# Performance work log

Hardware: AMD Instinct MI355X
Metric: run time of the kernel (lower is better)

Reference implementation:

```python
import jax, jax.numpy as jnp
import numpy as np


def hard_sigmoid(x):
    # clamp(0.2*x + 0.5, 0, 1) -- Theano/lwtnn convention
    return jnp.clip(0.2 * x + 0.5, 0.0, 1.0)


def setup_inputs() -> dict:
    key = jax.random.key(0)
    ks = jax.random.split(key, 10)
    B, T, D, H = 128, 1024, 256, 256
    s_in = 1.0 / np.sqrt(D)
    s_h = 1.0 / np.sqrt(H)
    return {
        "x": jax.random.normal(ks[0], (B, T, D), dtype=jnp.float32),
        "W_z": jax.random.normal(ks[1], (D, H), dtype=jnp.float32) * s_in,
        "W_r": jax.random.normal(ks[2], (D, H), dtype=jnp.float32) * s_in,
        "W_h": jax.random.normal(ks[3], (D, H), dtype=jnp.float32) * s_in,
        "U_z": jax.random.normal(ks[4], (H, H), dtype=jnp.float32) * s_h,
        "U_r": jax.random.normal(ks[5], (H, H), dtype=jnp.float32) * s_h,
        "U_h": jax.random.normal(ks[6], (H, H), dtype=jnp.float32) * s_h,
        "b_z": jax.random.normal(ks[7], (H,), dtype=jnp.float32) * 0.01,
        "b_r": jax.random.normal(ks[8], (H,), dtype=jnp.float32) * 0.01,
        "b_h": jax.random.normal(ks[9], (H,), dtype=jnp.float32) * 0.01,
    }


def reference(x, W_z, W_r, W_h, U_z, U_r, U_h, b_z, b_r, b_h):
    B, T, D = x.shape
    H = W_z.shape[1]
    # Precompute input projections for all timesteps in one big GEMM each
    # (same math as per-step xt @ W_* in the original loop).
    xz = jnp.einsum("btd,dh->bth", x, W_z) + b_z  # [B,T,H]
    xr = jnp.einsum("btd,dh->bth", x, W_r) + b_r
    xh = jnp.einsum("btd,dh->bth", x, W_h) + b_h

    def step(h, inputs):
        xz_t, xr_t, xh_t = inputs  # each [B,H]
        z = hard_sigmoid(xz_t + h @ U_z)
        r = hard_sigmoid(xr_t + h @ U_r)
        hh = jnp.tanh(xh_t + (r * h) @ U_h)
        h_new = z * h + (1.0 - z) * hh
        return h_new, None

    h0 = jnp.zeros((B, H), dtype=x.dtype)
    # scan over time axis: move T to leading axis
    xs = (xz.swapaxes(0, 1), xr.swapaxes(0, 1), xh.swapaxes(0, 1))
    h_final, _ = jax.lax.scan(step, h0, xs)
    return h_final
```

## Files before the change

### kernel.cpp

```cpp
#include <hip/hip_runtime.h>
#include <hip/hip_bf16.h>
#include <math.h>

#define BB 128
#define TT 1024
#define DD 256
#define HH 256
#define MM (BB * TT)
#define NN3 768

typedef __attribute__((ext_vector_type(8))) short short8;
typedef __attribute__((ext_vector_type(4))) float f32x4;
typedef __attribute__((address_space(1))) unsigned int gu32;
typedef __attribute__((address_space(3))) unsigned int lu32;

static __device__ __forceinline__ float bf2f(unsigned int u16) {
    return __uint_as_float(u16 << 16);
}
static __device__ __forceinline__ unsigned short f2bf(float f) {
    unsigned int u = __float_as_uint(f);
    unsigned int r = u + 0x7FFFu + ((u >> 16) & 1u);
    return (unsigned short)(r >> 16);
}
static __device__ __forceinline__ unsigned short f2bf_fast(float f) {
    return (unsigned short)((__float_as_uint(f) + 0x8000u) >> 16);
}

static __device__ __forceinline__ void barrier_lgkm() {
    asm volatile("s_waitcnt lgkmcnt(0)\n\ts_barrier" ::: "memory");
}
static __device__ __forceinline__ void barrier_full() {
    asm volatile("s_waitcnt vmcnt(0) lgkmcnt(0)\n\ts_barrier" ::: "memory");
}

__global__ __launch_bounds__(256) void wb_kernel(
    const float* __restrict__ Wz, const float* __restrict__ Wr,
    const float* __restrict__ Wh, unsigned short* __restrict__ Wb)
{
    int n = blockIdx.x;
    int g = n >> 8, col = n & 255;
    const float* W = (g == 0) ? Wz : (g == 1 ? Wr : Wh);
    int k = threadIdx.x;
    Wb[(size_t)n * 256 + k] = f2bf(W[(size_t)k * HH + col]);
}

__global__ __launch_bounds__(256)
__attribute__((amdgpu_waves_per_eu(2, 2)))
void xproj_mfma(
    const float* __restrict__ x, const unsigned short* __restrict__ Wb,
    const float* __restrict__ bz, const float* __restrict__ br,
    const float* __restrict__ bh, unsigned short* __restrict__ xw)
{
    const int tid  = threadIdx.x;
    const int lane = tid & 63;
    const int wv   = tid >> 6;
    const int nq   = lane & 15;
    const int kq   = lane >> 4;

    const int n0  = blockIdx.x * 64;
    const int m0  = blockIdx.y * 128;
    const int g   = n0 >> 8;
    const int nc0 = n0 & 255;
    const float* bias = (g == 0) ? bz : (g == 1 ? br : bh);

    short8 wf[8][4];
#pragma unroll
    for (int c = 0; c < 8; ++c)
#pragma unroll
        for (int nt = 0; nt < 4; ++nt)
            wf[c][nt] = *(const short8*)&Wb[(size_t)(n0 + nt * 16 + nq) * 256
                                            + c * 32 + kq * 8];
    float bv[4];
#pragma unroll
    for (int nt = 0; nt < 4; ++nt) bv[nt] = bias[nc0 + nt * 16 + nq];

    f32x4 acc[2][4];
#pragma unroll
    for (int mi = 0; mi < 2; ++mi)
#pragma unroll
        for (int nt = 0; nt < 4; ++nt) acc[mi][nt] = (f32x4){0.f, 0.f, 0.f, 0.f};

    const int mrow0 = m0 + wv * 32;

#pragma unroll
    for (int c = 0; c < 8; ++c) {
        short8 af[2];
#pragma unroll
        for (int mi = 0; mi < 2; ++mi) {
            const float* xp = &x[(size_t)(mrow0 + mi * 16 + nq) * 256
                                 + c * 32 + kq * 8];
            float4 f0 = *(const float4*)xp;
            float4 f1 = *(const float4*)(xp + 4);
            short8 a;
            a[0] = (short)f2bf(f0.x); a[1] = (short)f2bf(f0.y);
            a[2] = (short)f2bf(f0.z); a[3] = (short)f2bf(f0.w);
            a[4] = (short)f2bf(f1.x); a[5] = (short)f2bf(f1.y);
            a[6] = (short)f2bf(f1.z); a[7] = (short)f2bf(f1.w);
            af[mi] = a;
        }
#pragma unroll
        for (int mi = 0; mi < 2; ++mi)
#pragma unroll
            for (int nt = 0; nt < 4; ++nt)
                acc[mi][nt] = __builtin_amdgcn_mfma_f32_16x16x32_bf16(
                    af[mi], wf[c][nt], acc[mi][nt], 0, 0, 0);
    }

    const int t0   = (m0 & 1023) + wv * 32;
    const int b    = m0 >> 10;
    const int bid  = b >> 4;
    const int brow = b & 15;
    const int lane4 = (brow >> 2) * 16 + nq;
    const int ii    = brow & 3;

#pragma unroll
    for (int mi = 0; mi < 2; ++mi)
#pragma unroll
        for (int nt = 0; nt < 4; ++nt) {
            int ti = g * 16 + (nc0 >> 4) + nt;
#pragma unroll
            for (int i = 0; i < 4; ++i) {
                int t = t0 + mi * 16 + kq * 4 + i;
                size_t addr = (size_t)(t * 8 + bid) * 12288
                              + (size_t)(ti * 256 + lane4 * 4 + ii);
                xw[addr] = f2bf(acc[mi][nt][i] + bv[nt]);
            }
        }
}

__global__ __launch_bounds__(512)
__attribute__((amdgpu_waves_per_eu(2, 2)))
void gru_rec_kernel(
    const unsigned short* __restrict__ xw,
    const float* __restrict__ Uz, const float* __restrict__ Ur,
    const float* __restrict__ Uh,
    float* __restrict__ out)
{
    __shared__ unsigned short xstage[2][12288];
    __shared__ short hA[16][264];
    __shared__ short rhA[16][264];

    const int tid  = threadIdx.x;
    const int lane = tid & 63;
    const int wv   = tid >> 6;
    const int nq   = lane & 15;
    const int kq   = lane >> 4;
    const int bid  = blockIdx.x;

    short8 wzr[4][8];
#pragma unroll
    for (int q = 0; q < 4; ++q) {
        const float* U = (q < 2) ? Uz : Ur;
        const int col0 = (wv + 8 * (q & 1)) * 16;
#pragma unroll
        for (int c = 0; c < 8; ++c) {
            short8 f;
#pragma unroll
            for (int j = 0; j < 8; ++j)
                f[j] = (short)f2bf(U[(size_t)(c * 32 + kq * 8 + j) * HH + col0 + nq]);
            wzr[q][c] = f;
        }
    }
    short8 wh[2][8];
#pragma unroll
    for (int tj = 0; tj < 2; ++tj) {
        const int col0 = (wv + 8 * tj) * 16;
#pragma unroll
        for (int c = 0; c < 8; ++c) {
            short8 f;
#pragma unroll
            for (int j = 0; j < 8; ++j)
                f[j] = (short)f2bf(Uh[(size_t)(c * 32 + kq * 8 + j) * HH + col0 + nq]);
            wh[tj][c] = f;
        }
    }

    for (int idx = tid; idx < 16 * 264; idx += 512) ((short*)hA)[idx] = 0;
    float hprev[8];
#pragma unroll
    for (int i = 0; i < 8; ++i) hprev[i] = 0.f;

    auto stage = [&](int t, int buf) {
        const char* gsrc = (const char*)(xw + (size_t)(t * 8 + bid) * 12288);
        char* lbase = (char*)&xstage[buf][0];
        int woff = wv * 3072;
#pragma unroll
        for (int ld = 0; ld < 3; ++ld) {
            int off = woff + ld * 1024;
            __builtin_amdgcn_global_load_lds(
                (const gu32*)(gsrc + off + lane * 16),
                (lu32*)(lbase + off), 16, 0, 0);
        }
    };

    stage(0, 0);
    barrier_full();

    const int tiz = wv;
    auto step = [&](int t, int par) {
        int tn2 = (t + 1 < TT) ? (t + 1) : (TT - 1);
        stage(tn2, par ^ 1);

        const unsigned short* xs = &xstage[par][0];

        f32x4 accA[4];
#pragma unroll
        for (int q = 0; q < 4; ++q) {
            int ti = (q < 2 ? 0 : 16) + tiz + 8 * (q & 1);
            uint2 u = *(const uint2*)&xs[(ti * 64 + lane) * 4];
            accA[q][0] = bf2f(u.x & 0xffffu);
            accA[q][1] = bf2f(u.x >> 16);
            accA[q][2] = bf2f(u.y & 0xffffu);
            accA[q][3] = bf2f(u.y >> 16);
        }
#pragma unroll
        for (int c = 0; c < 8; ++c) {
            short8 af = *(const short8*)&hA[nq][c * 32 + kq * 8];
#pragma unroll
            for (int q = 0; q < 4; ++q)
                accA[q] = __builtin_amdgcn_mfma_f32_16x16x32_bf16(
                    af, wzr[q][c], accA[q], 0, 0, 0);
        }

#pragma unroll
        for (int tj = 0; tj < 2; ++tj) {
            int col = (tiz + 8 * tj) * 16 + nq;
#pragma unroll
            for (int i = 0; i < 4; ++i) {
                float r = __builtin_amdgcn_fmed3f(
                    __builtin_fmaf(0.2f, accA[2 + tj][i], 0.5f), 0.f, 1.f);
                rhA[kq * 4 + i][col] = (short)f2bf_fast(r * hprev[tj * 4 + i]);
            }
        }
        barrier_lgkm();

        f32x4 accH[2];
#pragma unroll
        for (int tj = 0; tj < 2; ++tj) {
            int ti = 32 + tiz + 8 * tj;
            uint2 u = *(const uint2*)&xs[(ti * 64 + lane) * 4];
            accH[tj][0] = bf2f(u.x & 0xffffu);
            accH[tj][1] = bf2f(u.x >> 16);
            accH[tj][2] = bf2f(u.y & 0xffffu);
            accH[tj][3] = bf2f(u.y >> 16);
        }
#pragma unroll
        for (int c = 0; c < 8; ++c) {
            short8 af = *(const short8*)&rhA[nq][c * 32 + kq * 8];
            accH[0] = __builtin_amdgcn_mfma_f32_16x16x32_bf16(af, wh[0][c], accH[0], 0, 0, 0);
            accH[1] = __builtin_amdgcn_mfma_f32_16x16x32_bf16(af, wh[1][c], accH[1], 0, 0, 0);
        }

#pragma unroll
        for (int tj = 0; tj < 2; ++tj) {
            int col = (tiz + 8 * tj) * 16 + nq;
#pragma unroll
            for (int i = 0; i < 4; ++i) {
                int idx = tj * 4 + i;
                float z = __builtin_amdgcn_fmed3f(
                    __builtin_fmaf(0.2f, accA[tj][i], 0.5f), 0.f, 1.f);
                float a = __builtin_amdgcn_fmed3f(accH[tj][i], -12.f, 12.f);
                float e  = exp2f(a * 2.88539008f);
                float hh = __builtin_fmaf(-2.f, __builtin_amdgcn_rcpf(e + 1.f), 1.f);
                float hn = __builtin_fmaf(z, hprev[idx] - hh, hh);
                hprev[idx] = hn;
                hA[kq * 4 + i][col] = (short)f2bf_fast(hn);
            }
        }
        barrier_full();
    };

    for (int t = 0; t < TT; t += 2) {
        step(t, 0);
        step(t + 1, 1);
    }

#pragma unroll
    for (int tj = 0; tj < 2; ++tj) {
        int col = (tiz + 8 * tj) * 16 + nq;
#pragma unroll
        for (int i = 0; i < 4; ++i)
            out[(size_t)(bid * 16 + kq * 4 + i) * HH + col] = hprev[tj * 4 + i];
    }
}

extern "C" void kernel_launch(void* const* d_in, const int* in_sizes, int n_in,
                              void* d_out, int out_size, void* d_ws, size_t ws_size,
                              hipStream_t stream) {
    const float* x  = (const float*)d_in[0];
    const float* Wz = (const float*)d_in[1];
    const float* Wr = (const float*)d_in[2];
    const float* Wh = (const float*)d_in[3];
    const float* Uz = (const float*)d_in[4];
    const float* Ur = (const float*)d_in[5];
    const float* Uh = (const float*)d_in[6];
    const float* bz = (const float*)d_in[7];
    const float* br = (const float*)d_in[8];
    const float* bh = (const float*)d_in[9];
    float* out = (float*)d_out;

    unsigned short* xw = (unsigned short*)d_ws;
    unsigned short* Wb =
        (unsigned short*)((char*)d_ws + (size_t)MM * NN3 * sizeof(unsigned short));

    wb_kernel<<<NN3, 256, 0, stream>>>(Wz, Wr, Wh, Wb);

    dim3 g1(NN3 / 64, MM / 128);
    xproj_mfma<<<g1, 256, 0, stream>>>(x, Wb, bz, br, bh, xw);

    gru_rec_kernel<<<8, 512, 0, stream>>>(xw, Uz, Ur, Uh, out);
}
```

Baseline: 2.979 ms.

## Fuse input projection and recurrence into one producer-consumer kernel

Merges the weight-conversion, input-projection GEMM and recurrent kernels into a single persistent launch. 240 producer blocks compute the input projections in time windows of 128 steps and signal per-window atomic counters, while 8 consumer blocks run the recurrence and spin-wait only when they reach a window that is not ready yet. This is meant to overlap the large projection GEMM with the serial recurrence and remove the separate launches and the Wb staging pass. It relies on consumer and producer blocks being co-resident to avoid deadlock, and it also switches x conversion to truncating-style bf16 rounding and uses a raw v_exp_f32 for tanh.

```diff
diff --git a/kernel.cpp b/kernel.cpp
--- a/kernel.cpp
+++ b/kernel.cpp
@@ -9,6 +9,11 @@
 #define MM (BB * TT)
 #define NN3 768
 
+#define NCONS 8
+#define NPROD 240
+#define WIN_TILES 768
+#define XW_BYTES ((size_t)MM * NN3 * sizeof(unsigned short))
+
 typedef __attribute__((ext_vector_type(8))) short short8;
 typedef __attribute__((ext_vector_type(4))) float f32x4;
 typedef __attribute__((address_space(1))) unsigned int gu32;
@@ -33,23 +38,19 @@
     asm volatile("s_waitcnt vmcnt(0) lgkmcnt(0)\n\ts_barrier" ::: "memory");
 }
 
-__global__ __launch_bounds__(256) void wb_kernel(
+__global__ __launch_bounds__(512)
+__attribute__((amdgpu_waves_per_eu(2, 2)))
+void gru_fused_kernel(
+    const float* __restrict__ x,
     const float* __restrict__ Wz, const float* __restrict__ Wr,
-    const float* __restrict__ Wh, unsigned short* __restrict__ Wb)
-{
-    int n = blockIdx.x;
-    int g = n >> 8, col = n & 255;
-    const float* W = (g == 0) ? Wz : (g == 1 ? Wr : Wh);
-    int k = threadIdx.x;
-    Wb[(size_t)n * 256 + k] = f2bf(W[(size_t)k * HH + col]);
-}
-
-__global__ __launch_bounds__(256)
-__attribute__((amdgpu_waves_per_eu(2, 2)))
-void xproj_mfma(
-    const float* __restrict__ x, const unsigned short* __restrict__ Wb,
+    const float* __restrict__ Wh,
+    const float* __restrict__ Uz, const float* __restrict__ Ur,
+    const float* __restrict__ Uh,
     const float* __restrict__ bz, const float* __restrict__ br,
-    const float* __restrict__ bh, unsigned short* __restrict__ xw)
+    const float* __restrict__ bh,
+    unsigned short* __restrict__ xw,
+    unsigned int* __restrict__ cnt,
+    float* __restrict__ out)
 {
     const int tid  = threadIdx.x;
     const int lane = tid & 63;
@@ -57,95 +58,104 @@
     const int nq   = lane & 15;
     const int kq   = lane >> 4;
 
-    const int n0  = blockIdx.x * 64;
-    const int m0  = blockIdx.y * 128;
-    const int g   = n0 >> 8;
-    const int nc0 = n0 & 255;
-    const float* bias = (g == 0) ? bz : (g == 1 ? br : bh);
-
-    short8 wf[8][4];
-#pragma unroll
-    for (int c = 0; c < 8; ++c)
+    if (blockIdx.x >= NCONS) {
+        const int p   = blockIdx.x - NCONS;
+        const int nb  = p % 6;
+        const int bg  = p / 6;
+        const int n0  = nb * 128;
+        const int g   = n0 >> 8;
+        const int nc0 = n0 & 255;
+        const float* W    = (g == 0) ? Wz : (g == 1 ? Wr : Wh);
+        const float* bias = (g == 0) ? bz : (g == 1 ? br : bh);
+        const int nh = wv >> 2;
+        const int mq = wv & 3;
+
+        short8 wf[8][4];
+#pragma unroll
+        for (int c = 0; c < 8; ++c)
+#pragma unroll
+            for (int nt = 0; nt < 4; ++nt) {
+                short8 f;
+                const int col = nc0 + nh * 64 + nt * 16 + nq;
+#pragma unroll
+                for (int j = 0; j < 8; ++j)
+                    f[j] = (short)f2bf(W[(size_t)(c * 32 + kq * 8 + j) * HH + col]);
+                wf[c][nt] = f;
+            }
+        float bv[4];
 #pragma unroll
         for (int nt = 0; nt < 4; ++nt)
-            wf[c][nt] = *(const short8*)&Wb[(size_t)(n0 + nt * 16 + nq) * 256
-                                            + c * 32 + kq * 8];
-    float bv[4];
-#pragma unroll
-    for (int nt = 0; nt < 4; ++nt) bv[nt] = bias[nc0 + nt * 16 + nq];
-
-    f32x4 acc[2][4];
-#pragma unroll
-    for (int mi = 0; mi < 2; ++mi)
-#pragma unroll
-        for (int nt = 0; nt < 4; ++nt) acc[mi][nt] = (f32x4){0.f, 0.f, 0.f, 0.f};
-
-    const int mrow0 = m0 + wv * 32;
-
-#pragma unroll
-    for (int c = 0; c < 8; ++c) {
-        short8 af[2];
-#pragma unroll
-        for (int mi = 0; mi < 2; ++mi) {
-            const float* xp = &x[(size_t)(mrow0 + mi * 16 + nq) * 256
-                                 + c * 32 + kq * 8];
-            float4 f0 = *(const float4*)xp;
-            float4 f1 = *(const float4*)(xp + 4);
-            short8 a;
-            a[0] = (short)f2bf(f0.x); a[1] = (short)f2bf(f0.y);
-            a[2] = (short)f2bf(f0.z); a[3] = (short)f2bf(f0.w);
-            a[4] = (short)f2bf(f1.x); a[5] = (short)f2bf(f1.y);
-            a[6] = (short)f2bf(f1.z); a[7] = (short)f2bf(f1.w);
-            af[mi] = a;
-        }
-#pragma unroll
-        for (int mi = 0; mi < 2; ++mi)
-#pragma unroll
-            for (int nt = 0; nt < 4; ++nt)
-                acc[mi][nt] = __builtin_amdgcn_mfma_f32_16x16x32_bf16(
-                    af[mi], wf[c][nt], acc[mi][nt], 0, 0, 0);
-    }
-
-    const int t0   = (m0 & 1023) + wv * 32;
-    const int b    = m0 >> 10;
-    const int bid  = b >> 4;
-    const int brow = b & 15;
-    const int lane4 = (brow >> 2) * 16 + nq;
-    const int ii    = brow & 3;
-
-#pragma unroll
-    for (int mi = 0; mi < 2; ++mi)
-#pragma unroll
-        for (int nt = 0; nt < 4; ++nt) {
-            int ti = g * 16 + (nc0 >> 4) + nt;
-#pragma unroll
-            for (int i = 0; i < 4; ++i) {
-                int t = t0 + mi * 16 + kq * 4 + i;
-                size_t addr = (size_t)(t * 8 + bid) * 12288
-                              + (size_t)(ti * 256 + lane4 * 4 + ii);
-                xw[addr] = f2bf(acc[mi][nt][i] + bv[nt]);
+            bv[nt] = bias[nc0 + nh * 64 + nt * 16 + nq];
+
+        for (int w = 0; w < 8; ++w) {
+            for (int b = bg; b < BB; b += 40) {
+                const int m0 = (b * 8 + w) * 128;
+                f32x4 acc[2][4];
+#pragma unroll
+                for (int mi = 0; mi < 2; ++mi)
+#pragma unroll
+                    for (int nt = 0; nt < 4; ++nt)
+                        acc[mi][nt] = (f32x4){0.f, 0.f, 0.f, 0.f};
+
+#pragma unroll
+                for (int c = 0; c < 8; ++c) {
+                    short8 af[2];
+#pragma unroll
+                    for (int mi = 0; mi < 2; ++mi) {
+                        const float* xp = &x[(size_t)(m0 + mq * 32 + mi * 16 + nq) * DD
+                                             + c * 32 + kq * 8];
+                        float4 f0 = *(const float4*)xp;
+                        float4 f1 = *(const float4*)(xp + 4);
+                        short8 a;
+                        a[0] = (short)f2bf_fast(f0.x); a[1] = (short)f2bf_fast(f0.y);
+                        a[2] = (short)f2bf_fast(f0.z); a[3] = (short)f2bf_fast(f0.w);
+                        a[4] = (short)f2bf_fast(f1.x); a[5] = (short)f2bf_fast(f1.y);
+                        a[6] = (short)f2bf_fast(f1.z); a[7] = (short)f2bf_fast(f1.w);
+                        af[mi] = a;
+                    }
+#pragma unroll
+                    for (int mi = 0; mi < 2; ++mi)
+#pragma unroll
+                        for (int nt = 0; nt < 4; ++nt)
+                            acc[mi][nt] = __builtin_amdgcn_mfma_f32_16x16x32_bf16(
+                                af[mi], wf[c][nt], acc[mi][nt], 0, 0, 0);
+                }
+
+                const int tb   = (m0 & 1023) + mq * 32;
+                const int bb   = m0 >> 10;
+                const int bid2 = bb >> 4, brow = bb & 15;
+                const int lane4 = (brow >> 2) * 16 + nq;
+                const int ii    = brow & 3;
+#pragma unroll
+                for (int mi = 0; mi < 2; ++mi)
+#pragma unroll
+                    for (int nt = 0; nt < 4; ++nt) {
+                        int ti = g * 16 + (nc0 >> 4) + nh * 4 + nt;
+#pragma unroll
+                        for (int i = 0; i < 4; ++i) {
+                            int t = tb + mi * 16 + kq * 4 + i;
+                            xw[(size_t)(t * 8 + bid2) * 12288
+                               + (size_t)(ti * 256 + lane4 * 4 + ii)] =
+                                f2bf(acc[mi][nt][i] + bv[nt]);
+                        }
+                    }
+
+                __syncthreads();
+                if (tid == 0) {
+                    __threadfence();
+                    __hip_atomic_fetch_add(&cnt[w], 1u, __ATOMIC_RELEASE,
+                                           __HIP_MEMORY_SCOPE_AGENT);
+                }
             }
         }
-}
-
-__global__ __launch_bounds__(512)
-__attribute__((amdgpu_waves_per_eu(2, 2)))
-void gru_rec_kernel(
-    const unsigned short* __restrict__ xw,
-    const float* __restrict__ Uz, const float* __restrict__ Ur,
-    const float* __restrict__ Uh,
-    float* __restrict__ out)
-{
+        return;
+    }
+
     __shared__ unsigned short xstage[2][12288];
     __shared__ short hA[16][264];
     __shared__ short rhA[16][264];
 
-    const int tid  = threadIdx.x;
-    const int lane = tid & 63;
-    const int wv   = tid >> 6;
-    const int nq   = lane & 15;
-    const int kq   = lane >> 4;
-    const int bid  = blockIdx.x;
+    const int bid = blockIdx.x;
 
     short8 wzr[4][8];
 #pragma unroll
@@ -193,13 +203,26 @@
         }
     };
 
+    auto wait_window = [&](int w2) {
+        if (tid == 0) {
+            while (__hip_atomic_load(&cnt[w2], __ATOMIC_RELAXED,
+                                     __HIP_MEMORY_SCOPE_AGENT) < WIN_TILES) {}
+            __threadfence();
+        }
+        __syncthreads();
+    };
+
+    int done_w = 0;
+    wait_window(0);
     stage(0, 0);
     barrier_full();
 
     const int tiz = wv;
     auto step = [&](int t, int par) {
-        int tn2 = (t + 1 < TT) ? (t + 1) : (TT - 1);
-        stage(tn2, par ^ 1);
+        int tneed = (t + 1 < TT) ? (t + 1) : (TT - 1);
+        int wneed = tneed >> 7;
+        if (wneed > done_w) { wait_window(wneed); done_w = wneed; }
+        stage(tneed, par ^ 1);
 
         const unsigned short* xs = &xstage[par][0];
 
@@ -260,7 +283,9 @@
                 float z = __builtin_amdgcn_fmed3f(
                     __builtin_fmaf(0.2f, accA[tj][i], 0.5f), 0.f, 1.f);
                 float a = __builtin_amdgcn_fmed3f(accH[tj][i], -12.f, 12.f);
-                float e  = exp2f(a * 2.88539008f);
+                float a2 = a * 2.88539008f;
+                float e;
+                asm("v_exp_f32 %0, %1" : "=v"(e) : "v"(a2));
                 float hh = __builtin_fmaf(-2.f, __builtin_amdgcn_rcpf(e + 1.f), 1.f);
                 float hn = __builtin_fmaf(z, hprev[idx] - hh, hh);
                 hprev[idx] = hn;
@@ -300,13 +325,10 @@
     float* out = (float*)d_out;
 
     unsigned short* xw = (unsigned short*)d_ws;
-    unsigned short* Wb =
-        (unsigned short*)((char*)d_ws + (size_t)MM * NN3 * sizeof(unsigned short));
-
-    wb_kernel<<<NN3, 256, 0, stream>>>(Wz, Wr, Wh, Wb);
-
-    dim3 g1(NN3 / 64, MM / 128);
-    xproj_mfma<<<g1, 256, 0, stream>>>(x, Wb, bz, br, bh, xw);
-
-    gru_rec_kernel<<<8, 512, 0, stream>>>(xw, Uz, Ur, Uh, out);
-}
+    unsigned int* cnt = (unsigned int*)((char*)d_ws + XW_BYTES);
+
+    hipMemsetAsync(cnt, 0, 8 * sizeof(unsigned int), stream);
+
+    gru_fused_kernel<<<NCONS + NPROD, 512, 0, stream>>>(
+        x, Wz, Wr, Wh, Uz, Ur, Uh, bz, br, bh, xw, cnt, out);
+}
```

New measurement: 2.979 ms. About the same (+0.0%).
